# Kernel optimization log

Hardware: AMD Instinct MI355X
Metric: run time of the kernel (lower is better)

Reference implementation:

```python
import jax, jax.numpy as jnp
import numpy as np

N_NODES = 100000
N_EDGES = 3200000
N_FEAT = 512
HIDDEN = 16
N_CLASSES = 64


def setup_inputs() -> dict:
    key = jax.random.key(0)
    k1, k2, k3, k4 = jax.random.split(key, 4)
    x = jax.random.normal(k1, (N_NODES, N_FEAT), dtype=jnp.float32)
    edge_index = jax.random.randint(k2, (2, N_EDGES), 0, N_NODES, dtype=jnp.int64)
    # Glorot-ish scaling keeps log_softmax numerically tame
    W1 = jax.random.normal(k3, (N_FEAT, HIDDEN), dtype=jnp.float32) / np.sqrt(N_FEAT)
    b1 = jnp.zeros((HIDDEN,), dtype=jnp.float32)
    W2 = jax.random.normal(k4, (HIDDEN, N_CLASSES), dtype=jnp.float32) / np.sqrt(HIDDEN)
    b2 = jnp.zeros((N_CLASSES,), dtype=jnp.float32)
    return {"x": x, "edge_index": edge_index, "W1": W1, "b1": b1, "W2": W2, "b2": b2}


def _gcn_conv(h, src, dst, norm, W, b, num_nodes):
    # dense transform first (PyG GCNConv order), then normalized scatter-add
    h = h @ W                                   # [N, out]
    msg = h[src] * norm[:, None]                # gather + edge scaling [E, out]
    agg = jax.ops.segment_sum(msg, dst, num_segments=num_nodes)
    return agg + b


def reference(x, edge_index, W1, b1, W2, b2):
    N = x.shape[0]
    loop = jnp.arange(N, dtype=edge_index.dtype)
    src = jnp.concatenate([edge_index[0], loop])  # add self-loops
    dst = jnp.concatenate([edge_index[1], loop])
    deg = jax.ops.segment_sum(jnp.ones_like(src, dtype=x.dtype), dst, num_segments=N)
    dinv = jax.lax.rsqrt(jnp.maximum(deg, 1.0))
    norm = dinv[src] * dinv[dst]                  # symmetric D^-1/2 A_hat D^-1/2

    h = jax.nn.relu(_gcn_conv(x, src, dst, norm, W1, b1, N))
    # dropout: identity in eval mode (training=False)
    h = _gcn_conv(h, src, dst, norm, W2, b2, N)
    return jax.nn.log_softmax(h, axis=1)
```

## Files before the change

### kernel.cpp

```cpp
#include <hip/hip_runtime.h>

#define NNODES 100000
#define NEDGES 3200000
#define NFEAT  512
#define NHID   16
#define NCLS   64
#define NB     391
#define CAP    10240
#define EPB    8192
#define GTPB   8
#define NGB    782

typedef short bf16x8 __attribute__((ext_vector_type(8)));
typedef float f32x4  __attribute__((ext_vector_type(4)));

__device__ __forceinline__ short f2bf(float f) {
    unsigned u = __float_as_uint(f);
    return (short)((u + 0x7FFFu + ((u >> 16) & 1u)) >> 16);
}
__device__ __forceinline__ float bf2f(unsigned short u) {
    return __uint_as_float((unsigned)u << 16);
}

struct PartShared {
    unsigned hist[NB];
    unsigned scn[512];
    unsigned cursor[NB];
    unsigned delta[NB];
    unsigned staged[EPB];
    unsigned short pbkt[EPB];
};
struct GemmShared { short w1t[16][520]; };
union FusedShared { PartShared p; GemmShared g; };

__global__ __launch_bounds__(512) void k_fused1(const int* __restrict__ src,
                                                const int* __restrict__ dst,
                                                unsigned* __restrict__ gcnt,
                                                unsigned* __restrict__ part,
                                                const float* __restrict__ x,
                                                const float* __restrict__ w1,
                                                unsigned short* __restrict__ hs1) {
    __shared__ FusedShared sh;
    int t = threadIdx.x;
    if (blockIdx.x < NB) {
        int base = blockIdx.x * EPB;
        int nblk = min(EPB, NEDGES - base);
        for (int i = t; i < NB; i += 512) sh.p.hist[i] = 0;
        __syncthreads();
        unsigned pk[16]; unsigned short bk[16];
#pragma unroll
        for (int j = 0; j < 16; ++j) {
            int o = t + j * 512;
            if (o < nblk) {
                int s = src[base + o], d = dst[base + o];
                pk[j] = (unsigned)s | ((unsigned)(d & 255) << 17);
                bk[j] = (unsigned short)(d >> 8);
                atomicAdd(&sh.p.hist[bk[j]], 1u);
            } else bk[j] = 0xFFFFu;
        }
        __syncthreads();
        sh.p.scn[t] = (t < NB) ? sh.p.hist[t] : 0u;
        __syncthreads();
#pragma unroll
        for (int off = 1; off < 512; off <<= 1) {
            unsigned a = (t >= off) ? sh.p.scn[t - off] : 0u;
            __syncthreads();
            sh.p.scn[t] += a;
            __syncthreads();
        }
        for (int i = t; i < NB; i += 512) {
            unsigned h = sh.p.hist[i];
            unsigned ex = sh.p.scn[i] - h;
            sh.p.cursor[i] = ex;
            unsigned gb = h ? atomicAdd(&gcnt[i], h) : 0u;
            sh.p.delta[i] = (unsigned)i * CAP + gb - ex;
        }
        __syncthreads();
#pragma unroll
        for (int j = 0; j < 16; ++j) {
            if (bk[j] != 0xFFFFu) {
                unsigned p = atomicAdd(&sh.p.cursor[bk[j]], 1u);
                sh.p.staged[p] = pk[j];
                sh.p.pbkt[p] = bk[j];
            }
        }
        __syncthreads();
        for (int i = t; i < nblk; i += 512) {
            unsigned b = sh.p.pbkt[i];
            unsigned d = sh.p.delta[b] + (unsigned)i;
            if (d < (b + 1u) * CAP) part[d] = sh.p.staged[i];
        }
    } else {
        for (int idx = t; idx < NFEAT * NHID; idx += 512) {
            int k = idx >> 4, n = idx & 15;
            sh.g.w1t[n][k] = f2bf(w1[idx]);
        }
        __syncthreads();
        int wave = t >> 6, lane = t & 63;
        int tile = (int)(blockIdx.x - NB) * GTPB + wave;
        if (tile >= NNODES / 16) return;
        int m = lane & 15, q = lane >> 4;
        const float* xrow = x + (size_t)(tile * 16 + m) * NFEAT + q * 8;
        const short* wrow = &sh.g.w1t[m][q * 8];
        f32x4 acc = {0.f, 0.f, 0.f, 0.f};
#pragma unroll
        for (int kb = 0; kb < NFEAT / 32; ++kb) {
            float4 a0 = *(const float4*)(xrow + kb * 32);
            float4 a1 = *(const float4*)(xrow + kb * 32 + 4);
            bf16x8 a;
            a[0] = f2bf(a0.x); a[1] = f2bf(a0.y); a[2] = f2bf(a0.z); a[3] = f2bf(a0.w);
            a[4] = f2bf(a1.x); a[5] = f2bf(a1.y); a[6] = f2bf(a1.z); a[7] = f2bf(a1.w);
            bf16x8 bfr = *(const bf16x8*)(wrow + kb * 32);
            acc = __builtin_amdgcn_mfma_f32_16x16x32_bf16(a, bfr, acc, 0, 0, 0);
        }
        unsigned short* outp = hs1 + (size_t)(tile * 16) * NHID;
#pragma unroll
        for (int r = 0; r < 4; ++r)
            outp[(q * 4 + r) * NHID + m] = (unsigned short)f2bf(acc[r]);
    }
}

__global__ __launch_bounds__(512) void k_scale(const unsigned* __restrict__ gcnt,
                                               const unsigned* __restrict__ part,
                                               float* __restrict__ dinv,
                                               unsigned short* __restrict__ hs1) {
    __shared__ unsigned hist[256];
    __shared__ float dl[256];
    int t = threadIdx.x, b = blockIdx.x;
    unsigned cb = min(gcnt[b], (unsigned)CAP);
    const unsigned* seg = part + (size_t)b * CAP;
    if (t < 256) hist[t] = 0;
    __syncthreads();
    for (unsigned i = t; i < cb; i += 512)
        atomicAdd(&hist[(seg[i] >> 17) & 255u], 1u);
    __syncthreads();
    if (t < 256) {
        dl[t] = rsqrtf((float)hist[t] + 1.f);
        int gn = b * 256 + t;
        if (gn < NNODES) dinv[gn] = dl[t];
    }
    __syncthreads();
    for (int i = t; i < 4096; i += 512) {
        int nd = i >> 4, ff = i & 15;
        int gn = b * 256 + nd;
        if (gn < NNODES) {
            size_t ix = (size_t)gn * NHID + ff;
            hs1[ix] = (unsigned short)f2bf(bf2f(hs1[ix]) * dl[nd]);
        }
    }
}

__global__ __launch_bounds__(512) void k_sortagg1(const unsigned* __restrict__ gcnt,
                                                  unsigned* __restrict__ part,
                                                  unsigned* __restrict__ offs,
                                                  unsigned* __restrict__ cnt,
                                                  const unsigned short* __restrict__ hs1,
                                                  const float* __restrict__ b1,
                                                  unsigned short* __restrict__ hs2) {
    __shared__ unsigned staged[CAP];
    __shared__ unsigned hist[256], cum[256], cur[256];
    __shared__ float dl[256];
    int t = threadIdx.x, b = blockIdx.x;
    int lane = t & 63, wv = t >> 6;
    int f = lane & 15, slot = lane >> 4;
    unsigned cb = min(gcnt[b], (unsigned)CAP);
    unsigned* seg = part + (size_t)b * CAP;
    if (t < 256) hist[t] = 0;
    __syncthreads();
    for (unsigned i = t; i < cb; i += 512)
        atomicAdd(&hist[(seg[i] >> 17) & 255u], 1u);
    __syncthreads();
    if (t < 256) cum[t] = hist[t];
    __syncthreads();
#pragma unroll
    for (int off = 1; off < 256; off <<= 1) {
        unsigned a = (t >= off && t < 256) ? cum[t - off] : 0u;
        __syncthreads();
        if (t < 256) cum[t] += a;
        __syncthreads();
    }
    if (t < 256) {
        unsigned ex = cum[t] - hist[t];
        cur[t] = ex;
        dl[t] = rsqrtf((float)hist[t] + 1.f);
        int node = b * 256 + t;
        if (node < NNODES) {
            offs[node] = (unsigned)b * CAP + ex;
            cnt[node] = hist[t];
        }
    }
    __syncthreads();
    for (unsigned i = t; i < cb; i += 512) {
        unsigned p = seg[i];
        unsigned r = atomicAdd(&cur[(p >> 17) & 255u], 1u);
        staged[r] = p & 0x1FFFFu;
    }
    __syncthreads();
    for (unsigned i = t; i < cb; i += 512)
        seg[i] = staged[i];
    float b1f = b1[f];
    for (int nd = wv; nd < 256; nd += 8) {
        int gn = b * 256 + nd;
        if (gn >= NNODES) continue;
        int lstart = (int)(cum[nd] - hist[nd]);
        int deg = (int)hist[nd];
        float di = dl[nd];
        float acc = 0.f;
        int rounds = (deg + 31) >> 5, cl = deg - 1;
        for (int r = 0; r < rounds; ++r) {
            int jb = r * 32 + slot * 8;
            unsigned e[8];
#pragma unroll
            for (int u = 0; u < 8; ++u) e[u] = staged[lstart + min(jb + u, cl)];
            float a[8];
#pragma unroll
            for (int u = 0; u < 8; ++u) a[u] = bf2f(hs1[(size_t)e[u] * NHID + f]);
#pragma unroll
            for (int u = 0; u < 8; ++u) acc += (jb + u < deg) ? a[u] : 0.f;
        }
        acc += __shfl_xor(acc, 16);
        acc += __shfl_xor(acc, 32);
        float v = (acc + bf2f(hs1[(size_t)gn * NHID + f])) * di + b1f;
        v = v > 0.f ? v : 0.f;
        if (slot == 0) hs2[(size_t)gn * NHID + f] = (unsigned short)f2bf(v * di);
    }
}

__global__ __launch_bounds__(256) void k_out2(const unsigned* __restrict__ offs,
                                              const unsigned* __restrict__ cnt,
                                              const unsigned* __restrict__ eb,
                                              const unsigned short* __restrict__ hs2,
                                              const float* __restrict__ dinv,
                                              const float* __restrict__ w2,
                                              const float* __restrict__ b2,
                                              float* __restrict__ out) {
    int tid = threadIdx.x;
    int node = blockIdx.x * 4 + (tid >> 6);
    int lane = tid & 63, f = lane & 15, slot = lane >> 4;
    unsigned start = offs[node];
    int deg = (int)cnt[node];
    float di = dinv[node];
    float w2c[NHID];
#pragma unroll
    for (int k = 0; k < NHID; ++k) w2c[k] = w2[k * NCLS + lane];
    float bb = b2[lane];
    float acc = 0.f;
    int rounds = (deg + 31) >> 5;
    int cl = deg - 1;
    for (int r = 0; r < rounds; ++r) {
        int jb = r * 32 + slot * 8;
        unsigned e[8];
#pragma unroll
        for (int u = 0; u < 8; ++u) e[u] = eb[start + min(jb + u, cl)];
        float a[8];
#pragma unroll
        for (int u = 0; u < 8; ++u) a[u] = bf2f(hs2[(size_t)e[u] * NHID + f]);
#pragma unroll
        for (int u = 0; u < 8; ++u) acc += (jb + u < deg) ? a[u] : 0.f;
    }
    acc += __shfl_xor(acc, 16);
    acc += __shfl_xor(acc, 32);
    float v = (acc + bf2f(hs2[(size_t)node * NHID + f])) * di;
    float logit = bb;
#pragma unroll
    for (int k = 0; k < NHID; ++k)
        logit += __shfl(v, k) * w2c[k];
    float mx = logit;
#pragma unroll
    for (int off = 32; off > 0; off >>= 1) mx = fmaxf(mx, __shfl_xor(mx, off));
    float ex = __expf(logit - mx);
    float s = ex;
#pragma unroll
    for (int off = 32; off > 0; off >>= 1) s += __shfl_xor(s, off);
    out[(size_t)node * NCLS + lane] = logit - mx - logf(s);
}

extern "C" void kernel_launch(void* const* d_in, const int* in_sizes, int n_in,
                              void* d_out, int out_size, void* d_ws, size_t ws_size,
                              hipStream_t stream) {
    const float* x  = (const float*)d_in[0];
    const int*   ei = (const int*)d_in[1];
    const float* w1 = (const float*)d_in[2];
    const float* b1 = (const float*)d_in[3];
    const float* w2 = (const float*)d_in[4];
    const float* b2 = (const float*)d_in[5];
    const int* src = ei;
    const int* dst = ei + NEDGES;

    char* ws = (char*)d_ws;
    unsigned* gcnt = (unsigned*)(ws + 0);
    unsigned* offs = (unsigned*)(ws + 2048);
    unsigned* cnt  = (unsigned*)(ws + 402048);
    float*    dinv = (float*)   (ws + 802048);
    unsigned short* hs1 = (unsigned short*)(ws + 1202048);
    unsigned short* hs2 = (unsigned short*)(ws + 4402048);
    unsigned* part = (unsigned*)(ws + 7602048);

    hipMemsetAsync(gcnt, 0, 2048, stream);
    k_fused1  <<<NB + NGB, 512, 0, stream>>>(src, dst, gcnt, part, x, w1, hs1);
    k_scale   <<<NB, 512, 0, stream>>>(gcnt, part, dinv, hs1);
    k_sortagg1<<<NB, 512, 0, stream>>>(gcnt, part, offs, cnt, hs1, b1, hs2);
    k_out2    <<<NNODES / 4, 256, 0, stream>>>(offs, cnt, part, hs2, dinv, w2, b2, (float*)d_out);
}
```

Baseline: 427.1 us.

## Vectorize neighbor row gathers via LDS transpose and batch nodes per wave in output kernel

Replaces per-feature 2-byte gathers of neighbor hidden rows with 16-byte loads where two lanes fetch one 32-byte row, staged through a padded per-wave LDS buffer and re-read so each lane sums two features. The same scheme is applied to the first aggregation and a new output kernel that processes 16 nodes per wave, amortizing the W2 register loads. It aims to cut memory instruction count and transaction overhead in the gather-bound aggregations, at the cost of extra LDS traffic and reliance on intra-wave ordering without explicit barriers.

```diff
diff --git a/kernel.cpp b/kernel.cpp
--- a/kernel.cpp
+++ b/kernel.cpp
@@ -160,9 +160,9 @@
     __shared__ unsigned staged[CAP];
     __shared__ unsigned hist[256], cum[256], cur[256];
     __shared__ float dl[256];
+    __shared__ __align__(16) unsigned char wrows[8][1536];
     int t = threadIdx.x, b = blockIdx.x;
     int lane = t & 63, wv = t >> 6;
-    int f = lane & 15, slot = lane >> 4;
     unsigned cb = min(gcnt[b], (unsigned)CAP);
     unsigned* seg = part + (size_t)b * CAP;
     if (t < 256) hist[t] = 0;
@@ -198,81 +198,109 @@
     __syncthreads();
     for (unsigned i = t; i < cb; i += 512)
         seg[i] = staged[i];
-    float b1f = b1[f];
+    int er = lane >> 1, half = lane & 1;
+    int c = lane & 7, g = lane >> 3;
+    unsigned char* wb = &wrows[wv][0];
+    float b1v0 = b1[2 * c], b1v1 = b1[2 * c + 1];
     for (int nd = wv; nd < 256; nd += 8) {
         int gn = b * 256 + nd;
         if (gn >= NNODES) continue;
         int lstart = (int)(cum[nd] - hist[nd]);
         int deg = (int)hist[nd];
         float di = dl[nd];
-        float acc = 0.f;
+        float v0 = 0.f, v1 = 0.f;
         int rounds = (deg + 31) >> 5, cl = deg - 1;
         for (int r = 0; r < rounds; ++r) {
-            int jb = r * 32 + slot * 8;
-            unsigned e[8];
-#pragma unroll
-            for (int u = 0; u < 8; ++u) e[u] = staged[lstart + min(jb + u, cl)];
-            float a[8];
-#pragma unroll
-            for (int u = 0; u < 8; ++u) a[u] = bf2f(hs1[(size_t)e[u] * NHID + f]);
-#pragma unroll
-            for (int u = 0; u < 8; ++u) acc += (jb + u < deg) ? a[u] : 0.f;
-        }
-        acc += __shfl_xor(acc, 16);
-        acc += __shfl_xor(acc, 32);
-        float v = (acc + bf2f(hs1[(size_t)gn * NHID + f])) * di + b1f;
-        v = v > 0.f ? v : 0.f;
-        if (slot == 0) hs2[(size_t)gn * NHID + f] = (unsigned short)f2bf(v * di);
-    }
-}
-
-__global__ __launch_bounds__(256) void k_out2(const unsigned* __restrict__ offs,
-                                              const unsigned* __restrict__ cnt,
-                                              const unsigned* __restrict__ eb,
-                                              const unsigned short* __restrict__ hs2,
-                                              const float* __restrict__ dinv,
-                                              const float* __restrict__ w2,
-                                              const float* __restrict__ b2,
-                                              float* __restrict__ out) {
-    int tid = threadIdx.x;
-    int node = blockIdx.x * 4 + (tid >> 6);
-    int lane = tid & 63, f = lane & 15, slot = lane >> 4;
-    unsigned start = offs[node];
-    int deg = (int)cnt[node];
-    float di = dinv[node];
+            int jb = r * 32;
+            unsigned e = staged[lstart + min(jb + er, cl)];
+            uint4 row = ((const uint4*)(hs1 + (size_t)e * NHID))[half];
+            *(uint4*)(wb + er * 48 + half * 16) = row;
+#pragma unroll
+            for (int k = 0; k < 4; ++k) {
+                int rr = g * 4 + k;
+                unsigned d = *(const unsigned*)(wb + rr * 48 + c * 4);
+                bool ok = (jb + rr) < deg;
+                v0 += ok ? bf2f((unsigned short)(d & 0xFFFFu)) : 0.f;
+                v1 += ok ? bf2f((unsigned short)(d >> 16)) : 0.f;
+            }
+        }
+        v0 += __shfl_xor(v0, 8);  v1 += __shfl_xor(v1, 8);
+        v0 += __shfl_xor(v0, 16); v1 += __shfl_xor(v1, 16);
+        v0 += __shfl_xor(v0, 32); v1 += __shfl_xor(v1, 32);
+        unsigned su = ((const unsigned*)(hs1 + (size_t)gn * NHID))[c];
+        float o0 = (v0 + bf2f((unsigned short)(su & 0xFFFFu))) * di + b1v0;
+        float o1 = (v1 + bf2f((unsigned short)(su >> 16))) * di + b1v1;
+        o0 = o0 > 0.f ? o0 : 0.f;
+        o1 = o1 > 0.f ? o1 : 0.f;
+        o0 *= di; o1 *= di;
+        unsigned pw = (unsigned)(unsigned short)f2bf(o0) |
+                      ((unsigned)(unsigned short)f2bf(o1) << 16);
+        if (lane < 8) ((unsigned*)(hs2 + (size_t)gn * NHID))[c] = pw;
+    }
+}
+
+__global__ __launch_bounds__(512) void k_out2v(const unsigned* __restrict__ offs,
+                                               const unsigned* __restrict__ cnt,
+                                               const unsigned* __restrict__ eb,
+                                               const unsigned short* __restrict__ hs2,
+                                               const float* __restrict__ dinv,
+                                               const float* __restrict__ w2,
+                                               const float* __restrict__ b2,
+                                               float* __restrict__ out) {
+    __shared__ __align__(16) unsigned char wrows[8][1536];
+    int t = threadIdx.x;
+    int lane = t & 63, wv = t >> 6;
+    int er = lane >> 1, half = lane & 1;
+    int c = lane & 7, g = lane >> 3;
+    unsigned char* wb = &wrows[wv][0];
     float w2c[NHID];
 #pragma unroll
     for (int k = 0; k < NHID; ++k) w2c[k] = w2[k * NCLS + lane];
     float bb = b2[lane];
-    float acc = 0.f;
-    int rounds = (deg + 31) >> 5;
-    int cl = deg - 1;
-    for (int r = 0; r < rounds; ++r) {
-        int jb = r * 32 + slot * 8;
-        unsigned e[8];
-#pragma unroll
-        for (int u = 0; u < 8; ++u) e[u] = eb[start + min(jb + u, cl)];
-        float a[8];
-#pragma unroll
-        for (int u = 0; u < 8; ++u) a[u] = bf2f(hs2[(size_t)e[u] * NHID + f]);
-#pragma unroll
-        for (int u = 0; u < 8; ++u) acc += (jb + u < deg) ? a[u] : 0.f;
-    }
-    acc += __shfl_xor(acc, 16);
-    acc += __shfl_xor(acc, 32);
-    float v = (acc + bf2f(hs2[(size_t)node * NHID + f])) * di;
-    float logit = bb;
-#pragma unroll
-    for (int k = 0; k < NHID; ++k)
-        logit += __shfl(v, k) * w2c[k];
-    float mx = logit;
-#pragma unroll
-    for (int off = 32; off > 0; off >>= 1) mx = fmaxf(mx, __shfl_xor(mx, off));
-    float ex = __expf(logit - mx);
-    float s = ex;
-#pragma unroll
-    for (int off = 32; off > 0; off >>= 1) s += __shfl_xor(s, off);
-    out[(size_t)node * NCLS + lane] = logit - mx - logf(s);
+    int nd0 = blockIdx.x * 128 + wv * 16;
+    for (int i = 0; i < 16; ++i) {
+        int gn = nd0 + i;
+        if (gn >= NNODES) break;
+        unsigned start = offs[gn];
+        int deg = (int)cnt[gn];
+        float di = dinv[gn];
+        float v0 = 0.f, v1 = 0.f;
+        int rounds = (deg + 31) >> 5, cl = deg - 1;
+        for (int r = 0; r < rounds; ++r) {
+            int jb = r * 32;
+            unsigned e = eb[start + min(jb + er, cl)];
+            uint4 row = ((const uint4*)(hs2 + (size_t)e * NHID))[half];
+            *(uint4*)(wb + er * 48 + half * 16) = row;
+#pragma unroll
+            for (int k = 0; k < 4; ++k) {
+                int rr = g * 4 + k;
+                unsigned d = *(const unsigned*)(wb + rr * 48 + c * 4);
+                bool ok = (jb + rr) < deg;
+                v0 += ok ? bf2f((unsigned short)(d & 0xFFFFu)) : 0.f;
+                v1 += ok ? bf2f((unsigned short)(d >> 16)) : 0.f;
+            }
+        }
+        v0 += __shfl_xor(v0, 8);  v1 += __shfl_xor(v1, 8);
+        v0 += __shfl_xor(v0, 16); v1 += __shfl_xor(v1, 16);
+        v0 += __shfl_xor(v0, 32); v1 += __shfl_xor(v1, 32);
+        unsigned su = ((const unsigned*)(hs2 + (size_t)gn * NHID))[c];
+        float t0 = (v0 + bf2f((unsigned short)(su & 0xFFFFu))) * di;
+        float t1 = (v1 + bf2f((unsigned short)(su >> 16))) * di;
+        float logit = bb;
+#pragma unroll
+        for (int k = 0; k < 8; ++k) {
+            logit += __shfl(t0, k) * w2c[2 * k];
+            logit += __shfl(t1, k) * w2c[2 * k + 1];
+        }
+        float mx = logit;
+#pragma unroll
+        for (int off = 32; off > 0; off >>= 1) mx = fmaxf(mx, __shfl_xor(mx, off));
+        float ex = __expf(logit - mx);
+        float s = ex;
+#pragma unroll
+        for (int off = 32; off > 0; off >>= 1) s += __shfl_xor(s, off);
+        out[(size_t)gn * NCLS + lane] = logit - mx - logf(s);
+    }
 }
 
 extern "C" void kernel_launch(void* const* d_in, const int* in_sizes, int n_in,
@@ -300,5 +328,5 @@
     k_fused1  <<<NB + NGB, 512, 0, stream>>>(src, dst, gcnt, part, x, w1, hs1);
     k_scale   <<<NB, 512, 0, stream>>>(gcnt, part, dinv, hs1);
     k_sortagg1<<<NB, 512, 0, stream>>>(gcnt, part, offs, cnt, hs1, b1, hs2);
-    k_out2    <<<NNODES / 4, 256, 0, stream>>>(offs, cnt, part, hs2, dinv, w2, b2, (float*)d_out);
-}
+    k_out2v   <<<(NNODES + 127) / 128, 512, 0, stream>>>(offs, cnt, part, hs2, dinv, w2, b2, (float*)d_out);
+}
```

Result: slower. 439.7 us (+2.9%).
